# Kernel optimization log

Measured on AMD Instinct MI355X. Metric: run time of the kernel, lower is better.

Reference implementation:

```python
import jax, jax.numpy as jnp
import numpy as np
import math

B, S, E, H, D, L, HF = 8, 1024, 512, 8, 64, 6, 2048
EPS = 1e-5
INF = 1000000.0


def _gelu(x):
    # custom tanh-approx gelu from the source
    return 0.5 * x * (1 + jnp.tanh(math.sqrt(2 / math.pi) * (x + 0.044715 * x ** 3)))


def _layernorm(x, gamma, beta):
    mean = jnp.mean(x, axis=-1, keepdims=True)
    var = jnp.mean((x - mean) ** 2, axis=-1, keepdims=True)
    return gamma * ((x - mean) / jnp.sqrt(var + EPS)) + beta


def setup_inputs() -> dict:
    key = jax.random.key(0)
    ks = jax.random.split(key, 10)
    scale = 0.02
    x = jax.random.normal(ks[0], (B, S, E), dtype=jnp.float32)
    att_mask = jax.random.randint(ks[1], (B, S), 0, 2) == 1
    WQ = jax.random.normal(ks[2], (L, E, E), dtype=jnp.float32) * scale
    WK = jax.random.normal(ks[3], (L, E, E), dtype=jnp.float32) * scale
    WV = jax.random.normal(ks[4], (L, E, E), dtype=jnp.float32) * scale
    WO = jax.random.normal(ks[5], (L, E, E), dtype=jnp.float32) * scale
    W1 = jax.random.normal(ks[6], (L, HF, E), dtype=jnp.float32) * scale
    W2 = jax.random.normal(ks[7], (L, E, HF), dtype=jnp.float32) * scale
    bQ = jnp.zeros((L, E)); bK = jnp.zeros((L, E)); bV = jnp.zeros((L, E)); bO = jnp.zeros((L, E))
    b1 = jnp.zeros((L, HF)); b2 = jnp.zeros((L, E))
    g1 = jnp.ones((L, E)); bt1 = jnp.zeros((L, E))
    g2 = jnp.ones((L, E)); bt2 = jnp.zeros((L, E))
    return {"x": x, "att_mask": att_mask, "WQ": WQ, "bQ": bQ, "WK": WK, "bK": bK,
            "WV": WV, "bV": bV, "WO": WO, "bO": bO, "W1": W1, "b1": b1, "W2": W2,
            "b2": b2, "g1": g1, "bt1": bt1, "g2": g2, "bt2": bt2}


def reference(x, att_mask, WQ, bQ, WK, bK, WV, bV, WO, bO, W1, b1, W2, b2, g1, bt1, g2, bt2):
    # additive mask applied to scores: score - (~mask) * infinity, broadcast over (B,1,1,S)
    inv_att = (~att_mask).astype(x.dtype)[:, None, None, :] * INF
    inv_sqrt_d = 1.0 / math.sqrt(D)
    for l in range(L):
        # --- multi-head self-attention ---
        q = (jnp.einsum('bse,fe->bsf', x, WQ[l]) + bQ[l]).reshape(B, S, H, D).transpose(0, 2, 1, 3)
        k = (jnp.einsum('bse,fe->bsf', x, WK[l]) + bK[l]).reshape(B, S, H, D).transpose(0, 2, 1, 3)
        v = (jnp.einsum('bse,fe->bsf', x, WV[l]) + bV[l]).reshape(B, S, H, D).transpose(0, 2, 1, 3)
        score = jnp.einsum('bhsd,bhtd->bhst', q, k) * inv_sqrt_d - inv_att
        attn = jax.nn.softmax(score, axis=-1)
        o = jnp.einsum('bhst,bhtd->bhsd', attn, v).transpose(0, 2, 1, 3).reshape(B, S, E)
        o = jnp.einsum('bse,fe->bsf', o, WO[l]) + bO[l]
        x = _layernorm(x + o, g1[l], bt1[l])
        # --- pointwise feed-forward ---
        h = _gelu(jnp.einsum('bse,fe->bsf', x, W1[l]) + b1[l])
        f = jnp.einsum('bsf,ef->bse', h, W2[l]) + b2[l]
        x = _layernorm(x + f, g2[l], bt2[l])
    return x
```

## Files before the change

kernel.cpp:

```cpp
#include <hip/hip_runtime.h>
#include <cstdint>
#include <cstddef>

#define NB 8
#define NS 1024
#define NE 512
#define NH 8
#define ND 64
#define NL 6
#define NHF 2048
#define NROW (NB*NS)

typedef __bf16 bf16_t;
typedef __bf16 bf8v __attribute__((ext_vector_type(8)));
typedef __bf16 bf4v __attribute__((ext_vector_type(4)));
typedef float  f4   __attribute__((ext_vector_type(4)));

extern "C" __device__ float __ocml_native_exp2_f32(float);
#define EXP2F __ocml_native_exp2_f32
#define LOG2E 1.4426950408889634f

__device__ __forceinline__ void async_copy16(const bf16_t* g, bf16_t* l) {
    __builtin_amdgcn_global_load_lds(
        (const __attribute__((address_space(1))) void*)g,
        (__attribute__((address_space(3))) void*)l,
        16, 0, 0);
}

__device__ __forceinline__ float gelu_f(float x) {
    const float s = fmaf(0.044715f * x * x, x, x);
    const float e = EXP2F(-2.3022081995f * s);
    return x * __builtin_amdgcn_rcpf(1.0f + e);
}

template<int BN, int ACT, int OUT>
__device__ __forceinline__ void gemm_core(
    bf16_t* __restrict__ sm,
    const bf16_t* __restrict__ A, const bf16_t* __restrict__ Bm,
    const float* __restrict__ bias, bf16_t* __restrict__ Cb,
    int m0, int n0, int N, int K)
{
    constexpr int JN = BN / 32, WSPAN = BN / 2;
    bf16_t* As = sm;
    bf16_t* Bs = sm + 2*128*64;
    const int tid  = threadIdx.x;
    const int lane = tid & 63;
    const int wave = tid >> 6;
    const int wm = wave >> 1, wn = wave & 1;
    const int quad = lane >> 4, l16 = lane & 15;
    const int srow = tid >> 3;
    const int scol = (((tid & 7) ^ (srow & 7)) << 3);

    f4 acc[4][JN] = {};

    const bf16_t* Ag = A  + (size_t)(m0 + srow) * K + scol;
    const bf16_t* Bg = Bm + (size_t)(n0 + srow) * K + scol;
    const int sw = (l16 & 7);

    auto stage = [&](int buf, int kt) {
#pragma unroll
        for (int r = 0; r < 4; ++r)
            async_copy16(Ag + (size_t)r * 32 * K + kt, As + buf*8192 + tid*8 + r*2048);
#pragma unroll
        for (int r = 0; r < BN/32; ++r)
            async_copy16(Bg + (size_t)r * 32 * K + kt, Bs + buf*(BN*64) + tid*8 + r*2048);
    };

    stage(0, 0);
    int buf = 0;
    for (int kt = 0; kt < K; kt += 64, buf ^= 1) {
        __syncthreads();
        if (kt + 64 < K) stage(buf ^ 1, kt + 64);
        const bf16_t* Ab = As + buf*8192;
        const bf16_t* Bb = Bs + buf*(BN*64);
#pragma unroll
        for (int s = 0; s < 2; ++s) {
            const int c8 = ((s*4 + quad) ^ sw) * 8;
            bf8v af[4], bfv[JN];
#pragma unroll
            for (int i = 0; i < 4; ++i)
                af[i] = *(const bf8v*)(Ab + (wm*64 + i*16 + l16)*64 + c8);
#pragma unroll
            for (int j = 0; j < JN; ++j)
                bfv[j] = *(const bf8v*)(Bb + (wn*WSPAN + j*16 + l16)*64 + c8);
#pragma unroll
            for (int i = 0; i < 4; ++i)
#pragma unroll
                for (int j = 0; j < JN; ++j) {
                    if (OUT == 3)
                        acc[i][j] = __builtin_amdgcn_mfma_f32_16x16x32_bf16(af[i], bfv[j], acc[i][j], 0, 0, 0);
                    else
                        acc[i][j] = __builtin_amdgcn_mfma_f32_16x16x32_bf16(bfv[j], af[i], acc[i][j], 0, 0, 0);
                }
        }
    }

    if (OUT != 3) {
#pragma unroll
        for (int i = 0; i < 4; ++i) {
            const size_t m = (size_t)(m0 + wm*64 + i*16 + l16);
#pragma unroll
            for (int j = 0; j < JN; ++j) {
                const int nb = n0 + wn*WSPAN + j*16 + quad*4;
                const f4 bv = *(const f4*)(bias + nb);
                f4 v = acc[i][j] + bv;
                if (ACT) {
#pragma unroll
                    for (int r = 0; r < 4; ++r) v[r] = gelu_f(v[r]);
                }
                bf4v* cp = (bf4v*)(Cb + m * (size_t)N + nb);
                bf4v o;
                if (OUT == 2) {
                    const bf4v old = *cp;
#pragma unroll
                    for (int r = 0; r < 4; ++r) o[r] = (bf16_t)((float)old[r] + v[r]);
                } else {
#pragma unroll
                    for (int r = 0; r < 4; ++r) o[r] = (bf16_t)v[r];
                }
                *cp = o;
            }
        }
    } else {
#pragma unroll
        for (int j = 0; j < JN; ++j) {
            const int n = n0 + wn*WSPAN + j*16 + l16;
            const float bv = bias[n];
#pragma unroll
            for (int i = 0; i < 4; ++i) {
                const int mbase = m0 + wm*64 + i*16 + quad*4;
                bf4v o;
#pragma unroll
                for (int r = 0; r < 4; ++r) o[r] = (bf16_t)(acc[i][j][r] + bv);
                const size_t b8h = (size_t)((mbase >> 10)*8 + (n >> 6));
                *(bf4v*)(Cb + (b8h*64 + (size_t)(n & 63))*1024 + (mbase & 1023)) = o;
            }
        }
    }
}

template<int BN, int ACT, int OUT>
__global__ __launch_bounds__(256)
void gemm_bt_k(const bf16_t* __restrict__ A, const bf16_t* __restrict__ Bm,
               const float* __restrict__ bias, bf16_t* __restrict__ Cb, int N, int K)
{
    __shared__ __align__(16) bf16_t smem[2*128*64 + 2*BN*64];
    gemm_core<BN, ACT, OUT>(smem, A, Bm, bias, Cb, blockIdx.x * 128, blockIdx.y * BN, N, K);
}

__global__ __launch_bounds__(256)
void gemm_qkv_k(const bf16_t* __restrict__ A,
                const bf16_t* __restrict__ wq, const bf16_t* __restrict__ wk, const bf16_t* __restrict__ wv,
                const float* __restrict__ bq, const float* __restrict__ bk, const float* __restrict__ bv,
                bf16_t* __restrict__ Q, bf16_t* __restrict__ K, bf16_t* __restrict__ Vt)
{
    __shared__ __align__(16) bf16_t smem[2*128*64 + 2*128*64];
    const int mat = blockIdx.y >> 2;
    const int m0 = blockIdx.x * 128, n0 = (blockIdx.y & 3) * 128;
    if (mat == 0)      gemm_core<128, 0, 1>(smem, A, wq, bq, Q,  m0, n0, NE, NE);
    else if (mat == 1) gemm_core<128, 0, 1>(smem, A, wk, bk, K,  m0, n0, NE, NE);
    else               gemm_core<128, 0, 3>(smem, A, wv, bv, Vt, m0, n0, NE, NE);
}

__global__ __launch_bounds__(256)
void attn_k(const bf16_t* __restrict__ Q, const bf16_t* __restrict__ Kg,
            const bf16_t* __restrict__ Vt, const float* __restrict__ maskf,
            bf16_t* __restrict__ O)
{
    __shared__ __align__(16) bf16_t Ks[2][64*64];
    __shared__ __align__(16) bf16_t Vs[2][64*64];
    __shared__ __align__(16) bf16_t Ps[4][32*64];
    const int tid  = threadIdx.x;
    const int lane = tid & 63;
    const int wave = tid >> 6;
    const int quad = lane >> 4, l16 = lane & 15;
    const int sw = l16 & 7;
    const int bh = blockIdx.x;
    const int b = bh >> 3, h = bh & 7;
    const int q0 = blockIdx.y * 128;

    bf8v qf[2][2];
#pragma unroll
    for (int qi = 0; qi < 2; ++qi) {
        const bf16_t* Qp = Q + (size_t)(b*NS + q0 + wave*32 + qi*16 + l16) * NE + h*ND;
        qf[qi][0] = *(const bf8v*)(Qp + quad*8);
        qf[qi][1] = *(const bf8v*)(Qp + 32 + quad*8);
    }

    f4 oacc[2][4] = {};
    float rs[2] = {0.f, 0.f};

    const int srow = tid >> 3;
    const int scol = (((tid & 7) ^ (srow & 7)) << 3);
    const float c1 = 0.125f * LOG2E;

    auto stage = [&](int buf, int kt) {
#pragma unroll
        for (int r = 0; r < 2; ++r) {
            async_copy16(Kg + (size_t)(b*NS + kt + r*32 + srow) * NE + h*ND + scol,
                         Ks[buf] + (r*256 + tid) * 8);
            async_copy16(Vt + (size_t)(bh*ND + r*32 + srow) * NS + kt + scol,
                         Vs[buf] + (r*256 + tid) * 8);
        }
    };

    stage(0, 0);
    int buf = 0;
    for (int kt = 0; kt < NS; kt += 64, buf ^= 1) {
        __syncthreads();
        if (kt + 64 < NS) stage(buf ^ 1, kt + 64);

        f4 sacc[2][4] = {};
#pragma unroll
        for (int j = 0; j < 4; ++j) {
            bf8v kf0 = *(const bf8v*)(Ks[buf] + (j*16 + l16)*64 + ((quad    ) ^ sw)*8);
            bf8v kf1 = *(const bf8v*)(Ks[buf] + (j*16 + l16)*64 + ((quad + 4) ^ sw)*8);
#pragma unroll
            for (int qi = 0; qi < 2; ++qi) {
                sacc[qi][j] = __builtin_amdgcn_mfma_f32_16x16x32_bf16(kf0, qf[qi][0], sacc[qi][j], 0, 0, 0);
                sacc[qi][j] = __builtin_amdgcn_mfma_f32_16x16x32_bf16(kf1, qf[qi][1], sacc[qi][j], 0, 0, 0);
            }
        }

        bf16_t* Pw = Ps[wave];
#pragma unroll
        for (int j = 0; j < 4; ++j) {
            const f4 mkv = *(const f4*)(maskf + b*NS + kt + j*16 + quad*4);
#pragma unroll
            for (int qi = 0; qi < 2; ++qi) {
                bf4v o;
#pragma unroll
                for (int r = 0; r < 4; ++r) {
                    const float p = EXP2F(fmaf(sacc[qi][j][r], c1, mkv[r]));
                    rs[qi] += p;
                    o[r] = (bf16_t)p;
                }
                const int row = qi*16 + l16;
                const int chunk = (j*2 + (quad >> 1)) ^ sw;
                *(bf4v*)(Pw + row*64 + chunk*8 + (quad & 1)*4) = o;
            }
        }

#pragma unroll
        for (int ks = 0; ks < 2; ++ks) {
            bf8v pf[2];
#pragma unroll
            for (int qi = 0; qi < 2; ++qi)
                pf[qi] = *(const bf8v*)(Pw + (qi*16 + l16)*64 + ((ks*4 + quad) ^ sw)*8);
#pragma unroll
            for (int nt = 0; nt < 4; ++nt) {
                bf8v vf = *(const bf8v*)(Vs[buf] + (nt*16 + l16)*64 + ((ks*4 + quad) ^ sw)*8);
#pragma unroll
                for (int qi = 0; qi < 2; ++qi)
                    oacc[qi][nt] = __builtin_amdgcn_mfma_f32_16x16x32_bf16(vf, pf[qi], oacc[qi][nt], 0, 0, 0);
            }
        }
    }

#pragma unroll
    for (int qi = 0; qi < 2; ++qi) {
        float s = rs[qi];
        s += __shfl_xor(s, 16, 64);
        s += __shfl_xor(s, 32, 64);
        const float inv = 1.0f / s;
        const size_t row = (size_t)(b*NS + q0 + wave*32 + qi*16 + l16);
#pragma unroll
        for (int nt = 0; nt < 4; ++nt) {
            bf4v o;
#pragma unroll
            for (int r = 0; r < 4; ++r) o[r] = (bf16_t)(oacc[qi][nt][r] * inv);
            *(bf4v*)(O + row * NE + h*ND + nt*16 + quad*4) = o;
        }
    }
}

__global__ __launch_bounds__(256)
void ln_k(bf16_t* __restrict__ xb,
          const float* __restrict__ gamma, const float* __restrict__ beta,
          float* __restrict__ fout, int wf)
{
    const int row = blockIdx.x;
    const int tid = threadIdx.x;
    const size_t base = (size_t)row * NE;
    const float x0 = (float)xb[base + tid];
    const float x1 = (float)xb[base + tid + 256];
    float s  = x0 + x1;
    float ss = x0*x0 + x1*x1;
#pragma unroll
    for (int off = 32; off > 0; off >>= 1) {
        s  += __shfl_down(s,  off, 64);
        ss += __shfl_down(ss, off, 64);
    }
    __shared__ float red[8];
    const int wave = tid >> 6;
    if ((tid & 63) == 0) { red[wave] = s; red[4 + wave] = ss; }
    __syncthreads();
    s  = red[0] + red[1] + red[2] + red[3];
    ss = red[4] + red[5] + red[6] + red[7];
    const float mean = s * (1.0f / NE);
    const float var  = ss * (1.0f / NE) - mean * mean;
    const float inv  = rsqrtf(var + 1e-5f);
    const float o0 = gamma[tid]       * ((x0 - mean) * inv) + beta[tid];
    const float o1 = gamma[tid + 256] * ((x1 - mean) * inv) + beta[tid + 256];
    xb[base + tid]       = (bf16_t)o0;
    xb[base + tid + 256] = (bf16_t)o1;
    if (wf) {
        fout[base + tid]       = o0;
        fout[base + tid + 256] = o1;
    }
}

#define W4SZ ((size_t)NL*NE*NE/4)
#define WBSZ ((size_t)NL*NE*NHF/4)
#define XSZ  ((size_t)NROW*NE/4)
#define CVT_TOTAL (4*W4SZ + 2*WBSZ + XSZ)

__global__ void cvt_all(const float* __restrict__ wq, const float* __restrict__ wk,
                        const float* __restrict__ wv, const float* __restrict__ wo,
                        const float* __restrict__ w1, const float* __restrict__ w2,
                        const float* __restrict__ x,
                        bf16_t* __restrict__ owq, bf16_t* __restrict__ owk,
                        bf16_t* __restrict__ owv, bf16_t* __restrict__ owo,
                        bf16_t* __restrict__ ow1, bf16_t* __restrict__ ow2,
                        bf16_t* __restrict__ ox)
{
    size_t i = (size_t)blockIdx.x * 256 + threadIdx.x;
    if (i >= CVT_TOTAL) return;
    const float* src; bf16_t* dst;
    if      (i < 1*W4SZ)           { src = wq; dst = owq; }
    else if (i < 2*W4SZ)           { src = wk; dst = owk; i -= 1*W4SZ; }
    else if (i < 3*W4SZ)           { src = wv; dst = owv; i -= 2*W4SZ; }
    else if (i < 4*W4SZ)           { src = wo; dst = owo; i -= 3*W4SZ; }
    else if (i < 4*W4SZ + WBSZ)    { src = w1; dst = ow1; i -= 4*W4SZ; }
    else if (i < 4*W4SZ + 2*WBSZ)  { src = w2; dst = ow2; i -= 4*W4SZ + WBSZ; }
    else                           { src = x;  dst = ox;  i -= 4*W4SZ + 2*WBSZ; }
    const f4 v = ((const f4*)src)[i];
    bf4v o;
    o[0] = (bf16_t)v[0]; o[1] = (bf16_t)v[1]; o[2] = (bf16_t)v[2]; o[3] = (bf16_t)v[3];
    ((bf4v*)dst)[i] = o;
}

__global__ void make_maskf(const int* __restrict__ m, float* __restrict__ out, int n)
{
    const int i = blockIdx.x * 256 + threadIdx.x;
    if (i < n) out[i] = m[i] ? 0.0f : -1.0e6f * LOG2E;
}

extern "C" void kernel_launch(void* const* d_in, const int* in_sizes, int n_in,
                              void* d_out, int out_size, void* d_ws, size_t ws_size,
                              hipStream_t stream)
{
    (void)in_sizes; (void)n_in; (void)out_size; (void)ws_size;
    const float* x   = (const float*)d_in[0];
    const int*   msk = (const int*)d_in[1];
    const float* WQ = (const float*)d_in[2];  const float* bQ  = (const float*)d_in[3];
    const float* WK = (const float*)d_in[4];  const float* bK  = (const float*)d_in[5];
    const float* WV = (const float*)d_in[6];  const float* bV  = (const float*)d_in[7];
    const float* WO = (const float*)d_in[8];  const float* bO  = (const float*)d_in[9];
    const float* W1 = (const float*)d_in[10]; const float* b1  = (const float*)d_in[11];
    const float* W2 = (const float*)d_in[12]; const float* b2  = (const float*)d_in[13];
    const float* g1 = (const float*)d_in[14]; const float* bt1 = (const float*)d_in[15];
    const float* g2 = (const float*)d_in[16]; const float* bt2 = (const float*)d_in[17];

    char* ws = (char*)d_ws;
    size_t off = 0;
    auto alloc = [&](size_t bytes) { char* p = ws + off; off += (bytes + 255) & ~(size_t)255; return p; };
    bf16_t* xb    = (bf16_t*)alloc((size_t)NROW*NE*2);
    bf16_t* Qb    = (bf16_t*)alloc((size_t)NROW*NE*2);
    bf16_t* Kb    = (bf16_t*)alloc((size_t)NROW*NE*2);
    bf16_t* Vtb   = (bf16_t*)alloc((size_t)NROW*NE*2);
    bf16_t* AOb   = (bf16_t*)alloc((size_t)NROW*NE*2);
    bf16_t* hb    = (bf16_t*)alloc((size_t)NROW*NHF*2);
    bf16_t* wqc   = (bf16_t*)alloc((size_t)NL*NE*NE*2);
    bf16_t* wkc   = (bf16_t*)alloc((size_t)NL*NE*NE*2);
    bf16_t* wvc   = (bf16_t*)alloc((size_t)NL*NE*NE*2);
    bf16_t* woc   = (bf16_t*)alloc((size_t)NL*NE*NE*2);
    bf16_t* w1c   = (bf16_t*)alloc((size_t)NL*NHF*NE*2);
    bf16_t* w2c   = (bf16_t*)alloc((size_t)NL*NE*NHF*2);
    float*  maskf = (float*) alloc((size_t)NB*NS*4);

    cvt_all<<<dim3((unsigned)((CVT_TOTAL + 255) / 256)), dim3(256), 0, stream>>>(
        WQ, WK, WV, WO, W1, W2, x, wqc, wkc, wvc, woc, w1c, w2c, xb);
    make_maskf<<<dim3(32), dim3(256), 0, stream>>>(msk, maskf, NB*NS);

    for (int l = 0; l < NL; ++l) {
        const bf16_t* wq  = wqc + (size_t)l*NE*NE;
        const bf16_t* wk  = wkc + (size_t)l*NE*NE;
        const bf16_t* wv  = wvc + (size_t)l*NE*NE;
        const bf16_t* wo  = woc + (size_t)l*NE*NE;
        const bf16_t* w1p = w1c + (size_t)l*NHF*NE;
        const bf16_t* w2p = w2c + (size_t)l*NE*NHF;

        gemm_qkv_k<<<dim3(64, 12), dim3(256), 0, stream>>>(
            xb, wq, wk, wv, bQ + l*NE, bK + l*NE, bV + l*NE, Qb, Kb, Vtb);
        attn_k<<<dim3(64, 8), dim3(256), 0, stream>>>(Qb, Kb, Vtb, maskf, AOb);
        gemm_bt_k<64, 0, 2><<<dim3(64, 8), dim3(256), 0, stream>>>(
            AOb, wo, bO + l*NE, xb, NE, NE);
        ln_k<<<dim3(NROW), dim3(256), 0, stream>>>(
            xb, g1 + l*NE, bt1 + l*NE, nullptr, 0);
        gemm_bt_k<128, 1, 1><<<dim3(64, 16), dim3(256), 0, stream>>>(
            xb, w1p, b1 + l*NHF, hb, NHF, NE);
        gemm_bt_k<64, 0, 2><<<dim3(64, 8), dim3(256), 0, stream>>>(
            hb, w2p, b2 + l*NE, xb, NE, NHF);
        const int last = (l == NL - 1);
        ln_k<<<dim3(NROW), dim3(256), 0, stream>>>(
            xb, g2 + l*NE, bt2 + l*NE, (float*)d_out, last);
    }
}
```

Measured before the change: 967.8 us.

## Compact unmasked keys per batch and skip masked key tiles in attention

A new pack kernel ranks each batch's key positions so that unmasked keys come first. The K and V projection epilogues scatter rows into that compacted order. Attention then iterates only over key tiles up to the unmasked count rounded to 64, which removes the work on the roughly half of keys that are masked. The cost is scattered scalar stores in the K/Vt epilogues in place of vector stores, plus a small extra kernel.

```diff
diff --git a/kernel.cpp b/kernel.cpp
--- a/kernel.cpp
+++ b/kernel.cpp
@@ -38,6 +38,7 @@
     bf16_t* __restrict__ sm,
     const bf16_t* __restrict__ A, const bf16_t* __restrict__ Bm,
     const float* __restrict__ bias, bf16_t* __restrict__ Cb,
+    const unsigned short* __restrict__ rank,
     int m0, int n0, int N, int K)
 {
     constexpr int JN = BN / 32, WSPAN = BN / 2;
@@ -87,7 +88,7 @@
             for (int i = 0; i < 4; ++i)
 #pragma unroll
                 for (int j = 0; j < JN; ++j) {
-                    if (OUT == 3)
+                    if (OUT == 5)
                         acc[i][j] = __builtin_amdgcn_mfma_f32_16x16x32_bf16(af[i], bfv[j], acc[i][j], 0, 0, 0);
                     else
                         acc[i][j] = __builtin_amdgcn_mfma_f32_16x16x32_bf16(bfv[j], af[i], acc[i][j], 0, 0, 0);
@@ -95,10 +96,12 @@
         }
     }
 
-    if (OUT != 3) {
+    if (OUT != 5) {
 #pragma unroll
         for (int i = 0; i < 4; ++i) {
-            const size_t m = (size_t)(m0 + wm*64 + i*16 + l16);
+            const int mi = m0 + wm*64 + i*16 + l16;
+            size_t m = (size_t)mi;
+            if (OUT == 4) m = (size_t)((mi & ~1023) + (int)rank[mi]);
 #pragma unroll
             for (int j = 0; j < JN; ++j) {
                 const int nb = n0 + wn*WSPAN + j*16 + quad*4;
@@ -129,11 +132,11 @@
 #pragma unroll
             for (int i = 0; i < 4; ++i) {
                 const int mbase = m0 + wm*64 + i*16 + quad*4;
-                bf4v o;
-#pragma unroll
-                for (int r = 0; r < 4; ++r) o[r] = (bf16_t)(acc[i][j][r] + bv);
                 const size_t b8h = (size_t)((mbase >> 10)*8 + (n >> 6));
-                *(bf4v*)(Cb + (b8h*64 + (size_t)(n & 63))*1024 + (mbase & 1023)) = o;
+                bf16_t* rowp = Cb + (b8h*64 + (size_t)(n & 63))*1024;
+#pragma unroll
+                for (int r = 0; r < 4; ++r)
+                    rowp[rank[mbase + r]] = (bf16_t)(acc[i][j][r] + bv);
             }
         }
     }
@@ -145,27 +148,64 @@
                const float* __restrict__ bias, bf16_t* __restrict__ Cb, int N, int K)
 {
     __shared__ __align__(16) bf16_t smem[2*128*64 + 2*BN*64];
-    gemm_core<BN, ACT, OUT>(smem, A, Bm, bias, Cb, blockIdx.x * 128, blockIdx.y * BN, N, K);
+    gemm_core<BN, ACT, OUT>(smem, A, Bm, bias, Cb, nullptr,
+                            blockIdx.x * 128, blockIdx.y * BN, N, K);
 }
 
 __global__ __launch_bounds__(256)
 void gemm_qkv_k(const bf16_t* __restrict__ A,
                 const bf16_t* __restrict__ wq, const bf16_t* __restrict__ wk, const bf16_t* __restrict__ wv,
                 const float* __restrict__ bq, const float* __restrict__ bk, const float* __restrict__ bv,
-                bf16_t* __restrict__ Q, bf16_t* __restrict__ K, bf16_t* __restrict__ Vt)
+                bf16_t* __restrict__ Q, bf16_t* __restrict__ K, bf16_t* __restrict__ Vt,
+                const unsigned short* __restrict__ rank)
 {
     __shared__ __align__(16) bf16_t smem[2*128*64 + 2*128*64];
     const int mat = blockIdx.y >> 2;
     const int m0 = blockIdx.x * 128, n0 = (blockIdx.y & 3) * 128;
-    if (mat == 0)      gemm_core<128, 0, 1>(smem, A, wq, bq, Q,  m0, n0, NE, NE);
-    else if (mat == 1) gemm_core<128, 0, 1>(smem, A, wk, bk, K,  m0, n0, NE, NE);
-    else               gemm_core<128, 0, 3>(smem, A, wv, bv, Vt, m0, n0, NE, NE);
+    if (mat == 0)      gemm_core<128, 0, 1>(smem, A, wq, bq, Q,  nullptr, m0, n0, NE, NE);
+    else if (mat == 1) gemm_core<128, 0, 4>(smem, A, wk, bk, K,  rank,    m0, n0, NE, NE);
+    else               gemm_core<128, 0, 5>(smem, A, wv, bv, Vt, rank,    m0, n0, NE, NE);
+}
+
+__global__ __launch_bounds__(64)
+void pack_k(const int* __restrict__ m, unsigned short* __restrict__ rank,
+            int* __restrict__ cntpad, float* __restrict__ maskp)
+{
+    const int b = blockIdx.x, lane = threadIdx.x;
+    unsigned long long bals[16];
+    int cnt = 0;
+#pragma unroll
+    for (int c = 0; c < 16; ++c) {
+        const bool mk = m[b*NS + c*64 + lane] != 0;
+        bals[c] = __ballot(mk);
+        cnt += __popcll(bals[c]);
+    }
+    int u = 0, kk = 0;
+#pragma unroll
+    for (int c = 0; c < 16; ++c) {
+        const unsigned long long bal = bals[c];
+        const bool mk = (bal >> lane) & 1;
+        const int pu = __popcll(bal & ((1ull << lane) - 1));
+        const int r = mk ? (u + pu) : (cnt + kk + (lane - pu));
+        rank[b*NS + c*64 + lane] = (unsigned short)r;
+        const int cb = __popcll(bal);
+        u += cb; kk += 64 - cb;
+    }
+    if (lane == 0) {
+        int cp = (cnt + 63) & ~63;
+        cntpad[b] = cp < 64 ? 64 : cp;
+    }
+#pragma unroll
+    for (int c = 0; c < 16; ++c) {
+        const int j = c*64 + lane;
+        maskp[b*NS + j] = (j < cnt) ? 0.0f : -1.0e6f * LOG2E;
+    }
 }
 
 __global__ __launch_bounds__(256)
 void attn_k(const bf16_t* __restrict__ Q, const bf16_t* __restrict__ Kg,
             const bf16_t* __restrict__ Vt, const float* __restrict__ maskf,
-            bf16_t* __restrict__ O)
+            const int* __restrict__ cntpad, bf16_t* __restrict__ O)
 {
     __shared__ __align__(16) bf16_t Ks[2][64*64];
     __shared__ __align__(16) bf16_t Vs[2][64*64];
@@ -178,6 +218,7 @@
     const int bh = blockIdx.x;
     const int b = bh >> 3, h = bh & 7;
     const int q0 = blockIdx.y * 128;
+    const int kend = cntpad[b];
 
     bf8v qf[2][2];
 #pragma unroll
@@ -206,9 +247,9 @@
 
     stage(0, 0);
     int buf = 0;
-    for (int kt = 0; kt < NS; kt += 64, buf ^= 1) {
+    for (int kt = 0; kt < kend; kt += 64, buf ^= 1) {
         __syncthreads();
-        if (kt + 64 < NS) stage(buf ^ 1, kt + 64);
+        if (kt + 64 < kend) stage(buf ^ 1, kt + 64);
 
         f4 sacc[2][4] = {};
 #pragma unroll
@@ -340,12 +381,6 @@
     ((bf4v*)dst)[i] = o;
 }
 
-__global__ void make_maskf(const int* __restrict__ m, float* __restrict__ out, int n)
-{
-    const int i = blockIdx.x * 256 + threadIdx.x;
-    if (i < n) out[i] = m[i] ? 0.0f : -1.0e6f * LOG2E;
-}
-
 extern "C" void kernel_launch(void* const* d_in, const int* in_sizes, int n_in,
                               void* d_out, int out_size, void* d_ws, size_t ws_size,
                               hipStream_t stream)
@@ -377,11 +412,13 @@
     bf16_t* woc   = (bf16_t*)alloc((size_t)NL*NE*NE*2);
     bf16_t* w1c   = (bf16_t*)alloc((size_t)NL*NHF*NE*2);
     bf16_t* w2c   = (bf16_t*)alloc((size_t)NL*NE*NHF*2);
-    float*  maskf = (float*) alloc((size_t)NB*NS*4);
+    float*  maskp = (float*) alloc((size_t)NB*NS*4);
+    unsigned short* rankb = (unsigned short*)alloc((size_t)NB*NS*2);
+    int*    cntp  = (int*)   alloc(NB*4);
 
     cvt_all<<<dim3((unsigned)((CVT_TOTAL + 255) / 256)), dim3(256), 0, stream>>>(
         WQ, WK, WV, WO, W1, W2, x, wqc, wkc, wvc, woc, w1c, w2c, xb);
-    make_maskf<<<dim3(32), dim3(256), 0, stream>>>(msk, maskf, NB*NS);
+    pack_k<<<dim3(NB), dim3(64), 0, stream>>>(msk, rankb, cntp, maskp);
 
     for (int l = 0; l < NL; ++l) {
         const bf16_t* wq  = wqc + (size_t)l*NE*NE;
@@ -392,8 +429,8 @@
         const bf16_t* w2p = w2c + (size_t)l*NE*NHF;
 
         gemm_qkv_k<<<dim3(64, 12), dim3(256), 0, stream>>>(
-            xb, wq, wk, wv, bQ + l*NE, bK + l*NE, bV + l*NE, Qb, Kb, Vtb);
-        attn_k<<<dim3(64, 8), dim3(256), 0, stream>>>(Qb, Kb, Vtb, maskf, AOb);
+            xb, wq, wk, wv, bQ + l*NE, bK + l*NE, bV + l*NE, Qb, Kb, Vtb, rankb);
+        attn_k<<<dim3(64, 8), dim3(256), 0, stream>>>(Qb, Kb, Vtb, maskp, cntp, AOb);
         gemm_bt_k<64, 0, 2><<<dim3(64, 8), dim3(256), 0, stream>>>(
             AOb, wo, bO + l*NE, xb, NE, NE);
         ln_k<<<dim3(NROW), dim3(256), 0, stream>>>(
```

Result: faster. 928.0 us (-4.1%).
